# Optimization experiments

Hardware: AMD Instinct MI355X
Metric: run time of the kernel (lower is better)

Reference implementation:

```python
import jax, jax.numpy as jnp
import numpy as np

DIM = 768
HEADS = 12
HEAD_DIM = DIM // HEADS
SCALE = HEAD_DIM ** -0.5
B = 8
N = 2121   # 1 cls + 1600 + 400 + 100 + 20 text
NT = 20

# token ranges: cls [0,1), x0 [1,1601), x1 [1601,2001), x2 [2001,2101), t [2101,2121)
SLICES = {'cls': (0, 1), 'x0': (1, 1601), 'x1': (1601, 2001), 'x2': (2001, 2101), 't': (2101, 2121)}


def setup_inputs() -> dict:
    key = jax.random.key(0)
    k1, k2, k3, k4 = jax.random.split(key, 4)
    src = jax.random.normal(k1, (B, N, DIM), dtype=jnp.float32)
    visu_mask = jnp.zeros((B, 2101), dtype=bool)   # True = masked out
    text_mask = jnp.zeros((B, NT), dtype=bool)
    w_qkv = jax.random.normal(k2, (DIM, 3 * DIM), dtype=jnp.float32) * 0.02
    w_proj = jax.random.normal(k3, (DIM, DIM), dtype=jnp.float32) * 0.02
    b_proj = jax.random.normal(k4, (DIM,), dtype=jnp.float32) * 0.02
    return {'src': src, 'visu_mask': visu_mask, 'text_mask': text_mask,
            'w_qkv': w_qkv, 'w_proj': w_proj, 'b_proj': b_proj}


def _attn(q, k, v, mask):
    # q: [B,H,Nq,D], k/v: [B,H,Nk,D], mask: [B,Nk] bool (True = masked)
    scores = jnp.einsum('bhqd,bhkd->bhqk', q * SCALE, k)
    scores = jnp.where(mask[:, None, None, :], -jnp.inf, scores)
    p = jax.nn.softmax(scores, axis=-1)
    o = jnp.einsum('bhqk,bhkd->bhqd', p, v)          # [B,H,Nq,D]
    return o.transpose(0, 2, 1, 3).reshape(q.shape[0], q.shape[2], -1)  # [B,Nq,C]


def reference(src, visu_mask, text_mask, w_qkv, w_proj, b_proj):
    qkv = (src @ w_qkv).reshape(B, N, 3, HEADS, HEAD_DIM).transpose(2, 0, 3, 1, 4)
    q, k, v = qkv[0], qkv[1], qkv[2]                  # [B,H,N,D]

    def blk(t, lo, hi):
        return t[:, :, lo:hi, :]

    (c0, c1), (a0, a1), (b0, b1), (d0, d1), (t0, t1) = (
        SLICES['cls'], SLICES['x0'], SLICES['x1'], SLICES['x2'], SLICES['t'])

    x0_mask = visu_mask[:, a0:a1]
    x1_mask = visu_mask[:, b0:b1]
    x2_mask = visu_mask[:, d0:d1]
    full_mask = jnp.concatenate([visu_mask, text_mask], axis=1)   # [B, N]

    # cls attends to everything
    cls = _attn(blk(q, c0, c1), k, v, full_mask)
    # x2 attends to x0+x1+x2+t
    k_x2 = jnp.concatenate([blk(k, a0, a1), blk(k, b0, b1), blk(k, d0, d1), blk(k, t0, t1)], axis=2)
    v_x2 = jnp.concatenate([blk(v, a0, a1), blk(v, b0, b1), blk(v, d0, d1), blk(v, t0, t1)], axis=2)
    m_x2 = jnp.concatenate([x0_mask, x1_mask, x2_mask, text_mask], axis=1)
    x2 = _attn(blk(q, d0, d1), k_x2, v_x2, m_x2)
    # x1 attends to x0+x1+t
    k_x1 = jnp.concatenate([blk(k, a0, a1), blk(k, b0, b1), blk(k, t0, t1)], axis=2)
    v_x1 = jnp.concatenate([blk(v, a0, a1), blk(v, b0, b1), blk(v, t0, t1)], axis=2)
    m_x1 = jnp.concatenate([x0_mask, x1_mask, text_mask], axis=1)
    x1 = _attn(blk(q, b0, b1), k_x1, v_x1, m_x1)
    # x0 attends to x0+t
    k_x0 = jnp.concatenate([blk(k, a0, a1), blk(k, t0, t1)], axis=2)
    v_x0 = jnp.concatenate([blk(v, a0, a1), blk(v, t0, t1)], axis=2)
    m_x0 = jnp.concatenate([x0_mask, text_mask], axis=1)
    x0 = _attn(blk(q, a0, a1), k_x0, v_x0, m_x0)
    # text attends to everything
    t = _attn(blk(q, t0, t1), k, v, full_mask)

    x = jnp.concatenate([cls, x0, x1, x2, t], axis=1)
    return x @ w_proj + b_proj
```

## Files before the change

kernel.cpp:

```cpp
#include <hip/hip_runtime.h>
#include <stdint.h>

typedef short           bf16x8 __attribute__((ext_vector_type(8)));
typedef float           f32x4  __attribute__((ext_vector_type(4)));
typedef float           f32x16 __attribute__((ext_vector_type(16)));
typedef unsigned short  u16;
typedef u16             u16x8  __attribute__((ext_vector_type(8)));
typedef uint32_t        u32;
typedef unsigned long long u64;

#define NB    8
#define NSEQ  2121
#define NPAD  2176
#define MROWS 16968
#define MPAD  17024
#define NH    12

#if __has_builtin(__builtin_amdgcn_exp2f)
#define EXP2F(x) __builtin_amdgcn_exp2f(x)
#else
#define EXP2F(x) exp2f(x)
#endif

#define INVALID_S   (-90000.0f)

__device__ __forceinline__ u16 f2bf(float f) {
  uint32_t u = __float_as_uint(f);
  u += 0x7fffu + ((u >> 16) & 1u);
  return (u16)(u >> 16);
}

__device__ __forceinline__ void gld_lds16(const void* g, void* l) {
  __builtin_amdgcn_global_load_lds(
      (const __attribute__((address_space(1))) unsigned int*)g,
      (__attribute__((address_space(3))) unsigned int*)l, 16, 0, 0);
}

__global__ void transpose_cast(const float* __restrict__ in, u16* __restrict__ out,
                               int R, int C, int scale_cols, float scale)
{
  __shared__ float tile[32][33];
  const int c0 = blockIdx.x * 32, r0 = blockIdx.y * 32;
  const int tx = threadIdx.x, ty = threadIdx.y;
#pragma unroll
  for (int i = 0; i < 4; i++) {
    const int r = r0 + ty + i * 8;
    tile[ty + i * 8][tx] = in[(size_t)r * C + c0 + tx];
  }
  __syncthreads();
#pragma unroll
  for (int i = 0; i < 4; i++) {
    const int c = c0 + ty + i * 8;
    float v = tile[tx][ty + i * 8];
    if (c < scale_cols) v *= scale;
    out[(size_t)c * R + r0 + tx] = f2bf(v);
  }
}

__global__ __launch_bounds__(256) void cast_src_bf16(const float* __restrict__ in,
                                                     u16* __restrict__ out)
{
  const size_t i = ((size_t)blockIdx.x * 256 + threadIdx.x) * 8;
  float4 a = *(const float4*)(in + i);
  float4 b = *(const float4*)(in + i + 4);
  u16x8 t;
  t[0] = f2bf(a.x); t[1] = f2bf(a.y); t[2] = f2bf(a.z); t[3] = f2bf(a.w);
  t[4] = f2bf(b.x); t[5] = f2bf(b.y); t[6] = f2bf(b.z); t[7] = f2bf(b.w);
  *(u16x8*)(out + i) = t;
}

__global__ __launch_bounds__(256) void gemm_qkv_kernel(
    const u16* __restrict__ srcb, const u16* __restrict__ wt,
    u16* __restrict__ qk, u16* __restrict__ vt)
{
  __shared__ u16 Asf[128 * 32];
  __shared__ u16 Bsf[128 * 32];
  const int tid  = threadIdx.x;
  const int lane = tid & 63, wave = tid >> 6;
  const int wr = wave >> 1, wc = wave & 1;
  const int col = lane & 15, grp = lane >> 4;
  const int m0 = blockIdx.y * 128, n0 = blockIdx.x * 128;
  const int arow = tid >> 2, akoff = (tid & 3) * 8;

  const f32x4 fz = {0.f, 0.f, 0.f, 0.f};
  f32x4 acc[4][4];
#pragma unroll
  for (int i = 0; i < 4; i++)
#pragma unroll
    for (int j = 0; j < 4; j++) acc[i][j] = fz;

  const u16* ag = srcb + (size_t)(m0 + arow) * 768 + akoff;
  const u16* bg = wt   + (size_t)(n0 + arow) * 768 + akoff;
  u16* al = &Asf[wave * 512];
  u16* bl = &Bsf[wave * 512];

  for (int kb = 0; kb < 768; kb += 32) {
    __syncthreads();
    gld_lds16(ag + kb,                      al);
    gld_lds16(ag + kb + (size_t)64 * 768,   al + 2048);
    gld_lds16(bg + kb,                      bl);
    gld_lds16(bg + kb + (size_t)64 * 768,   bl + 2048);
    __syncthreads();

    bf16x8 af[4], bfr[4];
#pragma unroll
    for (int mt = 0; mt < 4; mt++) af[mt]  = *(const bf16x8*)&Asf[(wr * 64 + mt * 16 + col) * 32 + grp * 8];
#pragma unroll
    for (int nt = 0; nt < 4; nt++) bfr[nt] = *(const bf16x8*)&Bsf[(wc * 64 + nt * 16 + col) * 32 + grp * 8];
#pragma unroll
    for (int mt = 0; mt < 4; mt++)
#pragma unroll
      for (int nt = 0; nt < 4; nt++)
        acc[mt][nt] = __builtin_amdgcn_mfma_f32_16x16x32_bf16(af[mt], bfr[nt], acc[mt][nt], 0, 0, 0);
  }

#pragma unroll
  for (int mt = 0; mt < 4; mt++) {
#pragma unroll
    for (int r = 0; r < 4; r++) {
      const int mm = m0 + wr * 64 + mt * 16 + grp * 4 + r;
      if (mm >= MROWS) continue;
      const uint32_t bb = (uint32_t)mm / 2121u;
      const uint32_t nn = (uint32_t)mm - bb * 2121u;
#pragma unroll
      for (int nt = 0; nt < 4; nt++) {
        const int c = n0 + wc * 64 + nt * 16 + col;
        const u16 bits = f2bf(acc[mt][nt][r]);
        if (c < 1536) {
          qk[(size_t)mm * 1536 + c] = bits;
        } else {
          const int hd = c - 1536;
          const int h = hd >> 6, d = hd & 63;
          vt[((size_t)(bb * NH + h) * 64 + d) * NPAD + nn] = bits;
        }
      }
    }
  }
}

__global__ __launch_bounds__(256) void gemm_proj_kernel(
    const u16* __restrict__ A, const u16* __restrict__ Bt,
    const float* __restrict__ bias, float* __restrict__ out)
{
  __shared__ u16 Asf[128 * 32];
  __shared__ u16 Bsf[128 * 32];
  const int tid  = threadIdx.x;
  const int lane = tid & 63, wave = tid >> 6;
  const int wr = wave >> 1, wc = wave & 1;
  const int col = lane & 15, grp = lane >> 4;
  const int m0 = blockIdx.y * 128, n0 = blockIdx.x * 128;
  const int arow = tid >> 2, akoff = (tid & 3) * 8;

  const f32x4 fz = {0.f, 0.f, 0.f, 0.f};
  f32x4 acc[4][4];
#pragma unroll
  for (int i = 0; i < 4; i++)
#pragma unroll
    for (int j = 0; j < 4; j++) acc[i][j] = fz;

  const u16* ag = A  + (size_t)(m0 + arow) * 768 + akoff;
  const u16* bg = Bt + (size_t)(n0 + arow) * 768 + akoff;
  u16* al = &Asf[wave * 512];
  u16* bl = &Bsf[wave * 512];

  for (int kb = 0; kb < 768; kb += 32) {
    __syncthreads();
    gld_lds16(ag + kb,                      al);
    gld_lds16(ag + kb + (size_t)64 * 768,   al + 2048);
    gld_lds16(bg + kb,                      bl);
    gld_lds16(bg + kb + (size_t)64 * 768,   bl + 2048);
    __syncthreads();

    bf16x8 af[4], bfr[4];
#pragma unroll
    for (int mt = 0; mt < 4; mt++) af[mt]  = *(const bf16x8*)&Asf[(wr * 64 + mt * 16 + col) * 32 + grp * 8];
#pragma unroll
    for (int nt = 0; nt < 4; nt++) bfr[nt] = *(const bf16x8*)&Bsf[(wc * 64 + nt * 16 + col) * 32 + grp * 8];
#pragma unroll
    for (int mt = 0; mt < 4; mt++)
#pragma unroll
      for (int nt = 0; nt < 4; nt++)
        acc[mt][nt] = __builtin_amdgcn_mfma_f32_16x16x32_bf16(af[mt], bfr[nt], acc[mt][nt], 0, 0, 0);
  }

#pragma unroll
  for (int mt = 0; mt < 4; mt++) {
#pragma unroll
    for (int r = 0; r < 4; r++) {
      const int mm = m0 + wr * 64 + mt * 16 + grp * 4 + r;
      if (mm >= MROWS) continue;
#pragma unroll
      for (int nt = 0; nt < 4; nt++) {
        const int c = n0 + wc * 64 + nt * 16 + col;
        out[(size_t)mm * 768 + c] = acc[mt][nt][r] + bias[c];
      }
    }
  }
}

__global__ __launch_bounds__(512) void attn_kernel(
    const u16* __restrict__ qkbuf, const u16* __restrict__ vt,
    const unsigned char* __restrict__ visu, const unsigned char* __restrict__ text,
    u16* __restrict__ attnout)
{
  __shared__ __align__(16) u16 Ks[2][64][72];
  __shared__ __align__(16) u16 Vs[2][64][72];
  __shared__ __align__(16) u64 mb64[34];
  __shared__ __align__(16) float lduf[8][32];

  const int tid  = threadIdx.x;
  const int lane = tid & 63, wave = tid >> 6;
  const int l31 = lane & 31, h = lane >> 5;

  const int fid = blockIdx.x;
  const int swz = (fid & 7) * 108 + (fid >> 3);
  const int qtile = swz % 9;
  const int bh = swz / 9;
  const int b = bh / NH, hh = bh % NH;
  const int qt0 = qtile * 256;
  const int q0 = qt0 + wave * 32;
  const int qrow = q0 + l31;

  for (int c = wave; c < 34; c += 8) {
    const int key = c * 64 + lane;
    int mb = 1;
    if (key < 2101)      mb = visu[b * 2101 + key] ? 1 : 0;
    else if (key < 2121) mb = text[b * 20 + (key - 2101)] ? 1 : 0;
    const u64 bal = __ballot(mb != 0);
    if (lane == 0) mb64[c] = bal;
  }

  const int qload = (qrow < NSEQ) ? qrow : (NSEQ - 1);
  bf16x8 qf[4];
  {
    const u16* qp = qkbuf + (size_t)(b * NSEQ + qload) * 1536 + hh * 64 + h * 8;
#pragma unroll
    for (int s = 0; s < 4; s++) qf[s] = *(const bf16x8*)(qp + s * 16);
  }

  int ks, ke, ex;
  if (qrow == 0)        { ks = 0; ke = 2121; ex = 0; }
  else if (qrow < 1601) { ks = 1; ke = 1601; ex = 1; }
  else if (qrow < 2001) { ks = 1; ke = 2001; ex = 1; }
  else if (qrow < 2101) { ks = 1; ke = 2121; ex = 0; }
  else if (qrow < 2121) { ks = 0; ke = 2121; ex = 0; }
  else                  { ks = 0; ke = 0;    ex = 0; }

  const int hi = (qt0 + 255 < 2120) ? (qt0 + 255) : 2120;
  int ke_tile, extra;
  if (qt0 == 0 || hi >= 2001) { ke_tile = 2121; extra = 0; }
  else if (hi >= 1601)        { ke_tile = 2001; extra = 1; }
  else                        { ke_tile = 1601; extra = 1; }
  const int nkv = (ke_tile + 63) >> 6;
  const int ntot = nkv + extra;

  f32x16 O0, O1;
#pragma unroll
  for (int i = 0; i < 16; i++) { O0[i] = 0.f; O1[i] = 0.f; }
  float lrun = 0.f;

  const int srow = tid >> 3, skoff = (tid & 7) * 8;
  const size_t vbase = (size_t)(b * NH + hh) * 64 * NPAD;
  const u16* kbase = qkbuf + (size_t)(b * NSEQ + srow) * 1536 + 768 + hh * 64 + skoff;
  const u16* vrow  = vt + vbase + (size_t)srow * NPAD + skoff;

  *(u16x8*)&Ks[0][srow][skoff] = *(const u16x8*)kbase;
  *(u16x8*)&Vs[0][srow][skoff] = *(const u16x8*)vrow;
  __syncthreads();

  u16x8 kpre, vpre;

  for (int it = 0; it < ntot; ++it) {
    const int cur = it & 1;
    const int kv0 = (it < nkv) ? it * 64 : 2096;
    const bool more = (it + 1 < ntot);

    if (more) {
      const int kvn = (it + 1 < nkv) ? (it + 1) * 64 : 2096;
      kpre = *(const u16x8*)(kbase + (size_t)kvn * 1536);
      vpre = *(const u16x8*)(vrow + kvn);
    }

    const int skipl = (kv0 >= ke) && !((ex != 0) && (kv0 < 2121) && (kv0 + 64 > 2101));
    if (!__all(skipl)) {
      f32x16 S0, S1;
#pragma unroll
      for (int i = 0; i < 16; i++) { S0[i] = 0.f; S1[i] = 0.f; }
      __builtin_amdgcn_s_setprio(1);
#pragma unroll
      for (int s = 0; s < 4; s++) {
        const bf16x8 k0 = *(const bf16x8*)&Ks[cur][l31][s * 16 + h * 8];
        const bf16x8 k1 = *(const bf16x8*)&Ks[cur][32 + l31][s * 16 + h * 8];
        S0 = __builtin_amdgcn_mfma_f32_32x32x16_bf16(k0, qf[s], S0, 0, 0, 0);
        S1 = __builtin_amdgcn_mfma_f32_32x32x16_bf16(k1, qf[s], S1, 0, 0, 0);
      }
      __builtin_amdgcn_s_setprio(0);

      const int fastl = (kv0 >= ks) && (kv0 + 64 <= ke);
      const u64 mword = (it < nkv) ? mb64[it] : ((mb64[32] >> 48) | (mb64[33] << 16));
      const bool plain = __all(fastl) && (mword == 0ull);
      if (!plain) {
        const u32 wlo = (u32)mword, whi = (u32)(mword >> 32);
#pragma unroll
        for (int m = 0; m < 4; m++) {
#pragma unroll
          for (int r = 0; r < 4; r++) {
            const int bitpos = 8 * m + 4 * h + r;
            {
              const int key = kv0 + bitpos;
              bool valid = ((key >= ks) && (key < ke)) || ((ex != 0) && (key >= 2101));
              valid = valid && (((wlo >> bitpos) & 1u) == 0u);
              S0[4 * m + r] = valid ? S0[4 * m + r] : INVALID_S;
            }
            {
              const int key = kv0 + 32 + bitpos;
              bool valid = ((key >= ks) && (key < ke)) || ((ex != 0) && (key >= 2101));
              valid = valid && (((whi >> bitpos) & 1u) == 0u);
              S1[4 * m + r] = valid ? S1[4 * m + r] : INVALID_S;
            }
          }
        }
      }

      float ls = 0.f;
#pragma unroll
      for (int i = 0; i < 16; i++) { const float p = EXP2F(S0[i]); S0[i] = p; ls += p; }
#pragma unroll
      for (int i = 0; i < 16; i++) { const float p = EXP2F(S1[i]); S1[i] = p; ls += p; }
      lrun += ls;

      bf16x8 pa[4];
      {
        u32 w[8];
#pragma unroll
        for (int j = 0; j < 8; j++) {
          u32 t;
          asm("v_cvt_pk_bf16_f32 %0, %1, %2" : "=v"(t) : "v"(S0[2 * j]), "v"(S0[2 * j + 1]));
          w[j] = t;
        }
        asm("v_permlane32_swap_b32 %0, %1" : "+v"(w[0]), "+v"(w[2]));
        asm("v_permlane32_swap_b32 %0, %1" : "+v"(w[1]), "+v"(w[3]));
        asm("v_permlane32_swap_b32 %0, %1" : "+v"(w[4]), "+v"(w[6]));
        asm("v_permlane32_swap_b32 %0, %1" : "+v"(w[5]), "+v"(w[7]));
        union { u32 u[4]; bf16x8 v; } f0, f1;
        f0.u[0] = w[0]; f0.u[1] = w[1]; f0.u[2] = w[2]; f0.u[3] = w[3];
        f1.u[0] = w[4]; f1.u[1] = w[5]; f1.u[2] = w[6]; f1.u[3] = w[7];
        pa[0] = f0.v; pa[1] = f1.v;
      }
      {
        u32 w[8];
#pragma unroll
        for (int j = 0; j < 8; j++) {
          u32 t;
          asm("v_cvt_pk_bf16_f32 %0, %1, %2" : "=v"(t) : "v"(S1[2 * j]), "v"(S1[2 * j + 1]));
          w[j] = t;
        }
        asm("v_permlane32_swap_b32 %0, %1" : "+v"(w[0]), "+v"(w[2]));
        asm("v_permlane32_swap_b32 %0, %1" : "+v"(w[1]), "+v"(w[3]));
        asm("v_permlane32_swap_b32 %0, %1" : "+v"(w[4]), "+v"(w[6]));
        asm("v_permlane32_swap_b32 %0, %1" : "+v"(w[5]), "+v"(w[7]));
        union { u32 u[4]; bf16x8 v; } f0, f1;
        f0.u[0] = w[0]; f0.u[1] = w[1]; f0.u[2] = w[2]; f0.u[3] = w[3];
        f1.u[0] = w[4]; f1.u[1] = w[5]; f1.u[2] = w[6]; f1.u[3] = w[7];
        pa[2] = f0.v; pa[3] = f1.v;
      }

      __builtin_amdgcn_s_setprio(1);
#pragma unroll
      for (int ck = 0; ck < 4; ck++) {
        const bf16x8 vf0 = *(const bf16x8*)&Vs[cur][l31][ck * 16 + h * 8];
        const bf16x8 vf1 = *(const bf16x8*)&Vs[cur][32 + l31][ck * 16 + h * 8];
        O0 = __builtin_amdgcn_mfma_f32_32x32x16_bf16(pa[ck], vf0, O0, 0, 0, 0);
        O1 = __builtin_amdgcn_mfma_f32_32x32x16_bf16(pa[ck], vf1, O1, 0, 0, 0);
      }
      __builtin_amdgcn_s_setprio(0);
    }

    if (more) {
      *(u16x8*)&Ks[cur ^ 1][srow][skoff] = kpre;
      *(u16x8*)&Vs[cur ^ 1][srow][skoff] = vpre;
    }
    __syncthreads();
  }

  float ltot = lrun + __shfl_xor(lrun, 32);
  if (h == 0) lduf[wave][l31] = ltot;
#pragma unroll
  for (int m = 0; m < 4; m++) {
    const f32x4 lv = *(const f32x4*)&lduf[wave][8 * m + 4 * h];
#pragma unroll
    for (int r = 0; r < 4; r++) {
      const float linv = (lv[r] > 0.f) ? 1.0f / lv[r] : 0.f;
      const int n = q0 + 8 * m + 4 * h + r;
      if (n >= NSEQ) continue;
      u16* op = attnout + (size_t)(b * NSEQ + n) * 768 + hh * 64 + l31;
      op[0]  = f2bf(O0[4 * m + r] * linv);
      op[32] = f2bf(O1[4 * m + r] * linv);
    }
  }
}

extern "C" void kernel_launch(void* const* d_in, const int* in_sizes, int n_in,
                              void* d_out, int out_size, void* d_ws, size_t ws_size,
                              hipStream_t stream) {
  const float* src  = (const float*)d_in[0];
  const unsigned char* visu = (const unsigned char*)d_in[1];
  const unsigned char* text = (const unsigned char*)d_in[2];
  const float* w_qkv = (const float*)d_in[3];
  const float* w_proj = (const float*)d_in[4];
  const float* b_proj = (const float*)d_in[5];
  float* out = (float*)d_out;

  char* ws = (char*)d_ws;
  size_t off = 0;
  auto alloc = [&](size_t bytes) { char* p = ws + off; off += (bytes + 255) & ~(size_t)255; return p; };
  u16* wqkv_t  = (u16*)alloc((size_t)2304 * 768 * 2);
  u16* wproj_t = (u16*)alloc((size_t)768 * 768 * 2);
  u16* qk      = (u16*)alloc((size_t)MPAD * 1536 * 2);
  u16* vtb     = (u16*)alloc((size_t)NB * NH * 64 * NPAD * 2);
  u16* tmp0    = (u16*)alloc((size_t)MPAD * 768 * 2);
  (void)ws_size; (void)in_sizes; (void)n_in; (void)out_size;

  transpose_cast<<<dim3(2304 / 32, 768 / 32), dim3(32, 8), 0, stream>>>(w_qkv, wqkv_t, 768, 2304, 768, 0.125f * 1.4426950408889634f);
  transpose_cast<<<dim3(768 / 32, 768 / 32), dim3(32, 8), 0, stream>>>(w_proj, wproj_t, 768, 768, 0, 1.0f);
  cast_src_bf16<<<dim3(6363), dim3(256), 0, stream>>>(src, tmp0);
  gemm_qkv_kernel<<<dim3(18, 133), dim3(256), 0, stream>>>(tmp0, wqkv_t, qk, vtb);
  attn_kernel<<<dim3(864), dim3(512), 0, stream>>>(qk, vtb, visu, text, tmp0);
  gemm_proj_kernel<<<dim3(6, 133), dim3(256), 0, stream>>>(tmp0, wproj_t, b_proj, out);
}
```

Measured before the change: 374.0 us.

## Load K/V tiles directly global-to-LDS with XOR-swizzled unpadded layout

Replaces register-staged K/V prefetch (global load into registers, then LDS store after compute) with direct global-to-LDS loads via gld_lds16 into unpadded 64x64 tiles. It uses an XOR swizzle on the 16-byte column slot to avoid bank conflicts, and also rewrites the row-sum of exp values as a tree reduction. The intent is to free VGPRs, remove the LDS store instructions, and shorten the dependent add chain. It relies on gld_lds16 being defined elsewhere and on async LDS writes being complete before the barrier.

After: 395.7 us. 1.06x slower.

```diff
diff --git a/kernel.cpp b/kernel.cpp
--- a/kernel.cpp
+++ b/kernel.cpp
@@ -203,8 +203,8 @@
     const unsigned char* __restrict__ visu, const unsigned char* __restrict__ text,
     u16* __restrict__ attnout)
 {
-  __shared__ __align__(16) u16 Ks[2][64][72];
-  __shared__ __align__(16) u16 Vs[2][64][72];
+  __shared__ __align__(16) u16 Ks2[2][64 * 64];
+  __shared__ __align__(16) u16 Vs2[2][64 * 64];
   __shared__ __align__(16) u64 mb64[34];
   __shared__ __align__(16) float lduf[8][32];
 
@@ -259,16 +259,15 @@
   for (int i = 0; i < 16; i++) { O0[i] = 0.f; O1[i] = 0.f; }
   float lrun = 0.f;
 
-  const int srow = tid >> 3, skoff = (tid & 7) * 8;
-  const size_t vbase = (size_t)(b * NH + hh) * 64 * NPAD;
-  const u16* kbase = qkbuf + (size_t)(b * NSEQ + srow) * 1536 + 768 + hh * 64 + skoff;
-  const u16* vrow  = vt + vbase + (size_t)srow * NPAD + skoff;
-
-  *(u16x8*)&Ks[0][srow][skoff] = *(const u16x8*)kbase;
-  *(u16x8*)&Vs[0][srow][skoff] = *(const u16x8*)vrow;
+  const int srow  = tid >> 3;
+  const int sslot = (tid & 7) ^ (srow & 7);
+  const u16* ksrc = qkbuf + (size_t)(b * NSEQ + srow) * 1536 + 768 + hh * 64 + sslot * 8;
+  const u16* vsrc = vt + (size_t)((b * NH + hh) * 64 + srow) * NPAD + sslot * 8;
+  const int x7 = l31 & 7;
+
+  gld_lds16(ksrc, &Ks2[0][wave * 512]);
+  gld_lds16(vsrc, &Vs2[0][wave * 512]);
   __syncthreads();
-
-  u16x8 kpre, vpre;
 
   for (int it = 0; it < ntot; ++it) {
     const int cur = it & 1;
@@ -277,8 +276,8 @@
 
     if (more) {
       const int kvn = (it + 1 < nkv) ? (it + 1) * 64 : 2096;
-      kpre = *(const u16x8*)(kbase + (size_t)kvn * 1536);
-      vpre = *(const u16x8*)(vrow + kvn);
+      gld_lds16(ksrc + (size_t)kvn * 1536, &Ks2[cur ^ 1][wave * 512]);
+      gld_lds16(vsrc + kvn,                &Vs2[cur ^ 1][wave * 512]);
     }
 
     const int skipl = (kv0 >= ke) && !((ex != 0) && (kv0 < 2121) && (kv0 + 64 > 2101));
@@ -289,8 +288,8 @@
       __builtin_amdgcn_s_setprio(1);
 #pragma unroll
       for (int s = 0; s < 4; s++) {
-        const bf16x8 k0 = *(const bf16x8*)&Ks[cur][l31][s * 16 + h * 8];
-        const bf16x8 k1 = *(const bf16x8*)&Ks[cur][32 + l31][s * 16 + h * 8];
+        const bf16x8 k0 = *(const bf16x8*)&Ks2[cur][l31 * 64        + ((s * 2 + h) ^ x7) * 8];
+        const bf16x8 k1 = *(const bf16x8*)&Ks2[cur][(32 + l31) * 64 + ((s * 2 + h) ^ x7) * 8];
         S0 = __builtin_amdgcn_mfma_f32_32x32x16_bf16(k0, qf[s], S0, 0, 0, 0);
         S1 = __builtin_amdgcn_mfma_f32_32x32x16_bf16(k1, qf[s], S1, 0, 0, 0);
       }
@@ -322,12 +321,21 @@
         }
       }
 
-      float ls = 0.f;
-#pragma unroll
-      for (int i = 0; i < 16; i++) { const float p = EXP2F(S0[i]); S0[i] = p; ls += p; }
-#pragma unroll
-      for (int i = 0; i < 16; i++) { const float p = EXP2F(S1[i]); S1[i] = p; ls += p; }
-      lrun += ls;
+#pragma unroll
+      for (int i = 0; i < 16; i++) S0[i] = EXP2F(S0[i]);
+#pragma unroll
+      for (int i = 0; i < 16; i++) S1[i] = EXP2F(S1[i]);
+      {
+        float a0 = (S0[0] + S0[1]) + (S0[2] + S0[3]);
+        float a1 = (S0[4] + S0[5]) + (S0[6] + S0[7]);
+        float a2 = (S0[8] + S0[9]) + (S0[10] + S0[11]);
+        float a3 = (S0[12] + S0[13]) + (S0[14] + S0[15]);
+        float b0 = (S1[0] + S1[1]) + (S1[2] + S1[3]);
+        float b1 = (S1[4] + S1[5]) + (S1[6] + S1[7]);
+        float b2 = (S1[8] + S1[9]) + (S1[10] + S1[11]);
+        float b3 = (S1[12] + S1[13]) + (S1[14] + S1[15]);
+        lrun += ((a0 + a1) + (a2 + a3)) + ((b0 + b1) + (b2 + b3));
+      }
 
       bf16x8 pa[4];
       {
@@ -368,18 +376,14 @@
       __builtin_amdgcn_s_setprio(1);
 #pragma unroll
       for (int ck = 0; ck < 4; ck++) {
-        const bf16x8 vf0 = *(const bf16x8*)&Vs[cur][l31][ck * 16 + h * 8];
-        const bf16x8 vf1 = *(const bf16x8*)&Vs[cur][32 + l31][ck * 16 + h * 8];
+        const bf16x8 vf0 = *(const bf16x8*)&Vs2[cur][l31 * 64        + ((ck * 2 + h) ^ x7) * 8];
+        const bf16x8 vf1 = *(const bf16x8*)&Vs2[cur][(32 + l31) * 64 + ((ck * 2 + h) ^ x7) * 8];
         O0 = __builtin_amdgcn_mfma_f32_32x32x16_bf16(pa[ck], vf0, O0, 0, 0, 0);
         O1 = __builtin_amdgcn_mfma_f32_32x32x16_bf16(pa[ck], vf1, O1, 0, 0, 0);
       }
       __builtin_amdgcn_s_setprio(0);
     }
 
-    if (more) {
-      *(u16x8*)&Ks[cur ^ 1][srow][skoff] = kpre;
-      *(u16x8*)&Vs[cur ^ 1][srow][skoff] = vpre;
-    }
     __syncthreads();
   }
 
```
